# Kernel tuning notes

Measured on AMD Instinct MI355X. Metric: run time of the kernel, lower is better.

## Reference

```python
import jax, jax.numpy as jnp
import numpy as np

NUM_HEADS = 4
LN_EPS = 1e-5
NEG_INF = -1e9


def _ln(x, g, b):
    mu = jnp.mean(x, axis=-1, keepdims=True)
    var = jnp.mean(jnp.square(x - mu), axis=-1, keepdims=True)
    return (x - mu) * jax.lax.rsqrt(var + LN_EPS) * g + b


def setup_inputs() -> dict:
    key = jax.random.key(0)
    B, L, D, C, E, T, H, NL, MLP = 1024, 200, 64, 32, 32, 8, 256, 3, 256
    P = D + E            # 96
    KIN = H + 2 * T      # 272
    ks = iter(jax.random.split(key, 64))

    def w(shape, fan_in):
        return jax.random.normal(next(ks), shape, dtype=jnp.float32) / np.sqrt(fan_in)

    inp = {}
    inp['x_u'] = jax.random.normal(next(ks), (B, D), dtype=jnp.float32)
    inp['x_ctx'] = jax.random.normal(next(ks), (B, L, D), dtype=jnp.float32)
    inp['t_ctx'] = jax.random.uniform(next(ks), (B, L), dtype=jnp.float32)
    inp['act_u_idx'] = jax.random.randint(next(ks), (B,), 0, C + 1)
    inp['act_ctx_idx'] = jax.random.randint(next(ks), (B, L), 0, C + 1)
    emb = jax.random.normal(next(ks), (C + 1, E), dtype=jnp.float32)
    inp['emb'] = emb.at[0].set(0.0)  # padding_idx=0
    inp['W_in_self'] = w((P, H), P); inp['b_in_self'] = jnp.zeros((H,), jnp.float32)
    inp['W_in_ctx'] = w((P, H), P); inp['b_in_ctx'] = jnp.zeros((H,), jnp.float32)
    inp['freq'] = jax.random.normal(next(ks), (NL, T), dtype=jnp.float32)
    inp['phase'] = jnp.zeros((NL, T), jnp.float32)
    inp['Wq'] = w((NL, H, H), H)
    inp['Wk'] = w((NL, KIN, H), KIN)
    inp['Wv'] = w((NL, KIN, H), KIN)
    inp['Wres'] = w((NL, H, H), H); inp['bres'] = jnp.zeros((NL, H), jnp.float32)
    inp['Wff1'] = w((NL, H, H), H); inp['bff1'] = jnp.zeros((NL, H), jnp.float32)
    inp['Wff2'] = w((NL, H, H), H); inp['bff2'] = jnp.zeros((NL, H), jnp.float32)
    inp['g1'] = jnp.ones((NL, H), jnp.float32); inp['beta1'] = jnp.zeros((NL, H), jnp.float32)
    inp['g2'] = jnp.ones((NL, H), jnp.float32); inp['beta2'] = jnp.zeros((NL, H), jnp.float32)
    inp['W_ro'] = w((H, MLP), H); inp['b_ro'] = jnp.zeros((MLP,), jnp.float32)
    inp['W_cls'] = w((MLP, C), MLP); inp['b_cls'] = jnp.zeros((C,), jnp.float32)
    inp['W_dt'] = w((MLP, 1), MLP); inp['b_dt'] = jnp.zeros((1,), jnp.float32)
    inp['W_rem'] = w((MLP, 1), MLP); inp['b_rem'] = jnp.zeros((1,), jnp.float32)
    return inp


def reference(x_u, x_ctx, t_ctx, act_u_idx, act_ctx_idx, emb,
              W_in_self, b_in_self, W_in_ctx, b_in_ctx,
              freq, phase, Wq, Wk, Wv, Wres, bres,
              Wff1, bff1, Wff2, bff2, g1, beta1, g2, beta2,
              W_ro, b_ro, W_cls, b_cls, W_dt, b_dt, W_rem, b_rem):
    B, L, _ = x_ctx.shape
    H = W_in_self.shape[1]
    nh = NUM_HEADS
    Dh = H // nh
    scale = np.sqrt(Dh).astype(np.float32)

    mask = act_ctx_idx > 0                                   # (B, L)
    e_u = emb[act_u_idx]                                     # (B, E)
    e_ctx = emb[act_ctx_idx]                                 # (B, L, E)
    xu = jnp.concatenate([x_u, e_u], axis=-1)
    xc = jnp.concatenate([x_ctx, e_ctx], axis=-1)
    h = xu @ W_in_self + b_in_self                           # (B, H)
    ctx = xc @ W_in_ctx + b_in_ctx                           # (B, L, H)

    logt = jnp.log1p(jnp.maximum(t_ctx, 0.0))                # (B, L)
    n_layers = Wq.shape[0]
    for i in range(n_layers):
        z = logt[..., None] * freq[i] + phase[i]             # (B, L, T)
        te = jnp.concatenate([jnp.sin(z), jnp.cos(z)], axis=-1)  # (B, L, 2T)
        kv = jnp.concatenate([ctx, te], axis=-1)             # (B, L, H+2T)
        q = (h @ Wq[i]).reshape(B, nh, Dh)                   # (B, h, d)
        k = (kv @ Wk[i]).reshape(B, L, nh, Dh)               # (B, l, h, d)
        v = (kv @ Wv[i]).reshape(B, L, nh, Dh)
        att_logits = jnp.einsum('bhd,blhd->bhl', q, k) / scale
        att_logits = jnp.where(mask[:, None, :], att_logits, NEG_INF)
        att = jax.nn.softmax(att_logits, axis=-1)            # (B, h, l)
        agg = jnp.einsum('bhl,blhd->bhd', att, v).reshape(B, H)
        z1 = _ln(agg + h @ Wres[i] + bres[i], g1[i], beta1[i])
        ff = jax.nn.relu(z1 @ Wff1[i] + bff1[i]) @ Wff2[i] + bff2[i]
        h = _ln(z1 + ff, g2[i], beta2[i])

    z = jax.nn.relu(h @ W_ro + b_ro)
    logits = z @ W_cls + b_cls
    dt_hat = jax.nn.sigmoid(z @ W_dt + b_dt)
    rem_hat = jax.nn.sigmoid(z @ W_rem + b_rem)
    return (logits, dt_hat, rem_hat)
```

## Files before the change

kernel.cpp:

```cpp
#include <hip/hip_runtime.h>
#include <math.h>

namespace {
constexpr int Bc   = 1024;
constexpr int Lc   = 200;
constexpr int Dc   = 64;
constexpr int Ec   = 32;
constexpr int Pc   = 96;
constexpr int Hc   = 256;
constexpr int Tc   = 8;
constexpr int NLc  = 3;
constexpr int KINc = 272;
constexpr int DHc  = 64;
constexpr int Cc   = 32;
constexpr int QS   = 113;
constexpr int Q4   = 452;
constexpr int QP   = 464;
constexpr int CG   = 112;
constexpr int CGW  = 448;
constexpr int XROWS = Bc * Lc + 8;
constexpr int TEBS  = Bc * Lc + 8;
constexpr float LN_EPS_V = 1e-5f;
constexpr float NEG_BIG  = -1e9f;

typedef __attribute__((ext_vector_type(8))) short bf16x8;
typedef __attribute__((ext_vector_type(4))) float f32x4;

__device__ __forceinline__ unsigned short f2bf(float f) {
    union { float f; unsigned int u; } v; v.f = f;
    unsigned int u = v.u;
    unsigned int r = (u + 0x7fffu + ((u >> 16) & 1u)) >> 16;
    return (unsigned short)r;
}
}

__global__ __launch_bounds__(256) void k_kpv(const float* __restrict__ W_in_ctx,
                                             const float* __restrict__ b_in_ctx,
                                             const float* __restrict__ Wv,
                                             const float* __restrict__ Wk,
                                             float* __restrict__ wvp2,
                                             float* __restrict__ kp) {
    int blk = blockIdx.x;
    int i = blk / QS;
    int j = blk - i * QS;
    int t = threadIdx.x;
    __shared__ float wrow[Hc];
    if (j < 96)        wrow[t] = W_in_ctx[j * Hc + t];
    else if (j == 112) wrow[t] = b_in_ctx[t];
    __syncthreads();
    const float* WvL = Wv + (size_t)i * KINc * Hc;
    const float* WkL = Wk + (size_t)i * KINc * Hc;
    float av, ak;
    if (j >= 96 && j < 112) {
        av = WvL[(256 + (j - 96)) * Hc + t];
        ak = WkL[(256 + (j - 96)) * Hc + t];
    } else {
        av = 0.f; ak = 0.f;
        for (int c = 0; c < Hc; ++c) {
            float w = wrow[c];
            av += w * WvL[c * Hc + t];
            ak += w * WkL[c * Hc + t];
        }
    }
    wvp2[(size_t)blk * Hc + t] = av;
    kp[(size_t)blk * Hc + t]   = ak;
}

__global__ __launch_bounds__(256) void k_wbig2(const float* __restrict__ Wq,
                                               const float* __restrict__ kp,
                                               float* __restrict__ wbig) {
    __shared__ float wq_l[64][65];
    __shared__ float kp_l[113][64];
    int blk = blockIdx.x;
    int i = blk >> 4;
    int rem = blk & 15;
    int h = rem >> 2, et = rem & 3;
    int t = threadIdx.x;
    for (int idx = t; idx < 64 * 64; idx += 256) {
        int e = idx >> 6, d = idx & 63;
        wq_l[e][d] = Wq[(size_t)i * Hc * Hc + (size_t)(et * 64 + e) * Hc + h * 64 + d];
    }
    for (int idx = t; idx < 113 * 64; idx += 256) {
        int r = idx >> 6, d = idx & 63;
        kp_l[r][d] = kp[((size_t)i * QS + r) * Hc + h * 64 + d];
    }
    __syncthreads();
    int e  = t & 63;
    int rq = t >> 6;
    for (int r = rq; r < QS; r += 4) {
        float acc = 0.f;
        #pragma unroll
        for (int d = 0; d < 64; ++d) acc += wq_l[e][d] * kp_l[r][d];
        wbig[((size_t)i * Hc + et * 64 + e) * Q4 + h * QS + r] = 0.125f * acc;
    }
}

__global__ __launch_bounds__(64) void k_frag(const float* __restrict__ wvp2,
                                             const float* __restrict__ Wres,
                                             const float* __restrict__ Wff1,
                                             const float* __restrict__ Wff2,
                                             const float* __restrict__ wbig,
                                             unsigned short* __restrict__ wcatF,
                                             unsigned short* __restrict__ wffF,
                                             unsigned short* __restrict__ wbigF) {
    int blk = blockIdx.x;
    int lane = threadIdx.x;
    unsigned short v[8];
    if (blk < NLc * 352) {
        int i = blk / 352;
        int r = blk - i * 352;
        int kk = r >> 4, ct = r & 15;
        int c = ct * 16 + (lane & 15);
        int kb = kk * 32 + (lane >> 4) * 8;
        #pragma unroll
        for (int j = 0; j < 8; ++j) {
            int k = kb + j;
            float val;
            if (k < 448) {
                int hh = k / 112, jj = k - hh * 112;
                val = ((c >> 6) == hh) ? wvp2[((size_t)i * QS + jj) * Hc + c] : 0.f;
            } else {
                val = Wres[(size_t)i * Hc * Hc + (k - 448) * Hc + c];
            }
            v[j] = f2bf(val);
        }
        *(uint4*)&wcatF[(size_t)blk * 64 * 8 + lane * 8] = *(const uint4*)v;
    } else if (blk < NLc * 352 + NLc * 256) {
        int b2 = blk - NLc * 352;
        int i = b2 / 256;
        int rem = b2 - i * 256;
        int w12 = rem >> 7;
        int r = rem & 127;
        int kk = r >> 4, ct = r & 15;
        int c = ct * 16 + (lane & 15);
        int kb = kk * 32 + (lane >> 4) * 8;
        const float* src = (w12 ? Wff2 : Wff1) + (size_t)i * Hc * Hc;
        #pragma unroll
        for (int j = 0; j < 8; ++j) v[j] = f2bf(src[(size_t)(kb + j) * Hc + c]);
        *(uint4*)&wffF[(size_t)b2 * 64 * 8 + lane * 8] = *(const uint4*)v;
    } else {
        int b3 = blk - NLc * 352 - NLc * 256;
        int i = b3 / 232;
        int r = b3 - i * 232;
        int kk = r / 29, ct = r - kk * 29;
        int c = ct * 16 + (lane & 15);
        int kb = kk * 32 + (lane >> 4) * 8;
        #pragma unroll
        for (int j = 0; j < 8; ++j) {
            float val = (c < Q4) ? wbig[((size_t)i * Hc + kb + j) * Q4 + c] : 0.f;
            v[j] = f2bf(val);
        }
        *(uint4*)&wbigF[(size_t)b3 * 64 * 8 + lane * 8] = *(const uint4*)v;
    }
}

__global__ __launch_bounds__(256) void k_h0(const float* __restrict__ x_u,
                                            const int* __restrict__ act_u,
                                            const float* __restrict__ emb,
                                            const float* __restrict__ W,
                                            const float* __restrict__ bias,
                                            float* __restrict__ h) {
    constexpr int R = 16;
    int b0 = blockIdx.x * R;
    int t = threadIdx.x;
    __shared__ float xu[R * Pc];
    for (int idx = t; idx < R * Pc; idx += 256) {
        int r = idx / Pc, j = idx - r * Pc;
        int b = b0 + r;
        float v;
        if (j < Dc) v = x_u[b * Dc + j];
        else        v = emb[act_u[b] * Ec + (j - Dc)];
        xu[idx] = v;
    }
    __syncthreads();
    float acc[R];
    float bb = bias[t];
    #pragma unroll
    for (int r = 0; r < R; ++r) acc[r] = bb;
    for (int j = 0; j < Pc; ++j) {
        float w = W[j * Hc + t];
        #pragma unroll
        for (int r = 0; r < R; ++r) acc[r] += xu[r * Pc + j] * w;
    }
    #pragma unroll
    for (int r = 0; r < R; ++r) h[(b0 + r) * Hc + t] = acc[r];
}

__global__ __launch_bounds__(256) void k_prepx(const float* __restrict__ x_ctx,
                                               const int* __restrict__ act_ctx,
                                               const float* __restrict__ emb,
                                               unsigned short* __restrict__ xtb,
                                               unsigned short* __restrict__ xtTb) {
    constexpr int ST2 = 116;
    __shared__ __align__(16) unsigned short xsT[96 * ST2];
    int blk = blockIdx.x;
    int b  = blk >> 1;
    int h0 = blk & 1;
    int t = threadIdx.x;
    int wv = t >> 6, lane = t & 63;
    int m = lane & 15, kg = lane >> 4;

    bf16x8 ifrag[2];
    #pragma unroll
    for (int hh = 0; hh < 2; ++hh) {
        unsigned short v[8];
        #pragma unroll
        for (int j8 = 0; j8 < 8; ++j8)
            v[j8] = (kg * 8 + j8 == m + 16 * hh) ? (unsigned short)0x3F80u : (unsigned short)0;
        ifrag[hh] = *(const bf16x8*)v;
    }

    for (int tile = wv; tile < 7; tile += 4) {
        int l = h0 * 112 + tile * 16 + m;
        bool valid = l < Lc;
        bf16x8 afr[3];
        #pragma unroll
        for (int kk = 0; kk < 2; ++kk) {
            unsigned short tmp[8];
            if (valid) {
                const float* s = x_ctx + ((size_t)(b * Lc + l)) * Dc + kk * 32 + kg * 8;
                float4 a0 = *(const float4*)s;
                float4 a1 = *(const float4*)(s + 4);
                tmp[0]=f2bf(a0.x); tmp[1]=f2bf(a0.y); tmp[2]=f2bf(a0.z); tmp[3]=f2bf(a0.w);
                tmp[4]=f2bf(a1.x); tmp[5]=f2bf(a1.y); tmp[6]=f2bf(a1.z); tmp[7]=f2bf(a1.w);
            } else {
                #pragma unroll
                for (int j = 0; j < 8; ++j) tmp[j] = 0;
            }
            afr[kk] = *(const bf16x8*)tmp;
        }
        {
            unsigned short tmp[8];
            if (valid) {
                int a = act_ctx[b * Lc + l];
                const float* s = emb + (size_t)a * Ec + kg * 8;
                float4 e0 = *(const float4*)s;
                float4 e1 = *(const float4*)(s + 4);
                tmp[0]=f2bf(e0.x); tmp[1]=f2bf(e0.y); tmp[2]=f2bf(e0.z); tmp[3]=f2bf(e0.w);
                tmp[4]=f2bf(e1.x); tmp[5]=f2bf(e1.y); tmp[6]=f2bf(e1.z); tmp[7]=f2bf(e1.w);
            } else {
                #pragma unroll
                for (int j = 0; j < 8; ++j) tmp[j] = 0;
            }
            afr[2] = *(const bf16x8*)tmp;
        }
        if (valid) {
            unsigned short* dst = xtb + ((size_t)(b * Lc + l)) * 96;
            *(uint4*)(dst + kg * 8)      = *(const uint4*)&afr[0];
            *(uint4*)(dst + 32 + kg * 8) = *(const uint4*)&afr[1];
            *(uint4*)(dst + 64 + kg * 8) = *(const uint4*)&afr[2];
        }
        #pragma unroll
        for (int kk = 0; kk < 3; ++kk) {
            #pragma unroll
            for (int hh = 0; hh < 2; ++hh) {
                f32x4 d = {0.f, 0.f, 0.f, 0.f};
                d = __builtin_amdgcn_mfma_f32_16x16x32_bf16(afr[kk], ifrag[hh], d, 0, 0, 0);
                int j  = kk * 32 + hh * 16 + m;
                int l0 = tile * 16 + kg * 4;
                unsigned int u0 = (unsigned int)f2bf(d[0]) | ((unsigned int)f2bf(d[1]) << 16);
                unsigned int u1 = (unsigned int)f2bf(d[2]) | ((unsigned int)f2bf(d[3]) << 16);
                uint2 uu; uu.x = u0; uu.y = u1;
                *(uint2*)&xsT[j * ST2 + l0] = uu;
            }
        }
    }
    __syncthreads();

    for (int idx = t; idx < 96 * 14; idx += 256) {
        int j = idx / 14, ch = idx - j * 14;
        uint2 a  = *(const uint2*)&xsT[j * ST2 + ch * 8];
        uint2 b2 = *(const uint2*)&xsT[j * ST2 + ch * 8 + 4];
        uint4 o; o.x = a.x; o.y = a.y; o.z = b2.x; o.w = b2.y;
        *(uint4*)&xtTb[((size_t)(b * 96 + j)) * 224 + h0 * 112 + ch * 8] = o;
    }
}

__global__ __launch_bounds__(256) void k_prept(const float* __restrict__ t_ctx,
                                               const float* __restrict__ freq,
                                               const float* __restrict__ phase,
                                               unsigned short* __restrict__ teb,
                                               unsigned short* __restrict__ teTb) {
    __shared__ float lt[Lc];
    int b = blockIdx.x;
    int t = threadIdx.x;
    if (t < Lc) lt[t] = log1pf(fmaxf(t_ctx[b * Lc + t], 0.f));
    __syncthreads();
    for (int idx = t; idx < NLc * Lc; idx += 256) {
        int i = idx / Lc, l = idx - i * Lc;
        float L = lt[l];
        unsigned short v[16];
        #pragma unroll
        for (int j = 0; j < 8; ++j) {
            float z = L * freq[i * Tc + j] + phase[i * Tc + j];
            v[j]     = f2bf(__sinf(z));
            v[8 + j] = f2bf(__cosf(z));
        }
        size_t base = ((size_t)i * TEBS + b * Lc + l) * 16;
        *(uint4*)&teb[base]     = *(const uint4*)v;
        *(uint4*)&teb[base + 8] = *(const uint4*)&v[8];
    }
    for (int idx = t; idx < NLc * 16 * 28; idx += 256) {
        int i  = idx / 448;
        int r2 = idx - i * 448;
        int f  = r2 / 28, ch = r2 - f * 28;
        int l0 = ch * 8;
        float fr = freq[i * Tc + (f & 7)], ph = phase[i * Tc + (f & 7)];
        bool iscos = f >= 8;
        unsigned short v[8];
        #pragma unroll
        for (int k = 0; k < 8; ++k) {
            int l = l0 + k;
            float val = 0.f;
            if (l < Lc) {
                float z = lt[l] * fr + ph;
                val = iscos ? __cosf(z) : __sinf(z);
            }
            v[k] = f2bf(val);
        }
        *(uint4*)&teTb[((size_t)i * Bc * 16 + b * 16 + f) * 224 + l0] = *(const uint4*)v;
    }
}

__global__ __launch_bounds__(256) void k_qk2b(const float* __restrict__ h,
                                              const float* __restrict__ wbig_l,
                                              unsigned short* __restrict__ qk2b) {
    constexpr int R = 4;
    int rb = blockIdx.x & 255;
    int cb = blockIdx.x >> 8;
    int b0 = rb * R;
    int t = threadIdx.x;
    int c = cb * 256 + t;
    __shared__ float hl[R * Hc];
    for (int idx = t; idx < R * Hc; idx += 256) hl[idx] = h[b0 * Hc + idx];
    __syncthreads();
    if (c >= QP) return;
    if (c >= Q4) {
        #pragma unroll
        for (int r = 0; r < R; ++r) qk2b[(size_t)(b0 + r) * QP + c] = 0;
        return;
    }
    float acc[R];
    #pragma unroll
    for (int r = 0; r < R; ++r) acc[r] = 0.f;
    for (int e = 0; e < Hc; ++e) {
        float w = wbig_l[(size_t)e * Q4 + c];
        #pragma unroll
        for (int r = 0; r < R; ++r) acc[r] += hl[r * Hc + e] * w;
    }
    #pragma unroll
    for (int r = 0; r < R; ++r) qk2b[(size_t)(b0 + r) * QP + c] = f2bf(acc[r]);
}

__global__ __launch_bounds__(512) void k_att(const int* __restrict__ act_ctx,
                                             const unsigned short* __restrict__ qk2b,
                                             const unsigned short* __restrict__ xtb,
                                             const unsigned short* __restrict__ xtTb,
                                             const unsigned short* __restrict__ teb_l,
                                             const unsigned short* __restrict__ teTb_l,
                                             float* __restrict__ cagg) {
    __shared__ unsigned short qks[QP];
    __shared__ float S[4][208];
    __shared__ unsigned short Pl[16][232];
    int b = blockIdx.x;
    int t = threadIdx.x;
    int wv = t >> 6, lane = t & 63;
    int kg = lane >> 4;

    if (t < QP / 2) ((unsigned int*)qks)[t] = ((const unsigned int*)(qk2b + (size_t)b * QP))[t];
    for (int idx = t; idx < 16 * 29; idx += 512) {
        int row = idx / 29, c8 = idx - row * 29;
        uint4 z = {0, 0, 0, 0};
        *(uint4*)&Pl[row][c8 * 8] = z;
    }
    __syncthreads();

    bf16x8 bfr[4];
    {
        int h = lane & 15;
        int kb = kg * 8;
        #pragma unroll
        for (int kk = 0; kk < 4; ++kk) {
            unsigned short tmp[8];
            #pragma unroll
            for (int j = 0; j < 8; ++j) {
                int k = kk * 32 + kb + j;
                tmp[j] = (h < 4 && k < QS) ? qks[h * QS + k] : (unsigned short)0;
            }
            bfr[kk] = *(const bf16x8*)tmp;
        }
    }

    const unsigned short* xrow  = xtb   + (size_t)b * Lc * 96;
    const unsigned short* terow = teb_l + (size_t)b * Lc * 16;
    for (int tile = wv; tile < 13; tile += 8) {
        int r = tile * 16 + (lane & 15);
        bf16x8 a0 = *(const bf16x8*)(xrow + (size_t)r * 96 + kg * 8);
        bf16x8 a1 = *(const bf16x8*)(xrow + (size_t)r * 96 + 32 + kg * 8);
        bf16x8 a2 = *(const bf16x8*)(xrow + (size_t)r * 96 + 64 + kg * 8);
        bf16x8 a3;
        if (kg < 2) {
            a3 = *(const bf16x8*)(terow + (size_t)r * 16 + kg * 8);
        } else if (kg == 2) {
            unsigned short tmp[8] = {0x3F80u, 0, 0, 0, 0, 0, 0, 0};
            a3 = *(const bf16x8*)tmp;
        } else {
            bf16x8 z = {0, 0, 0, 0, 0, 0, 0, 0};
            a3 = z;
        }
        f32x4 acc = {0.f, 0.f, 0.f, 0.f};
        acc = __builtin_amdgcn_mfma_f32_16x16x32_bf16(a0, bfr[0], acc, 0, 0, 0);
        acc = __builtin_amdgcn_mfma_f32_16x16x32_bf16(a1, bfr[1], acc, 0, 0, 0);
        acc = __builtin_amdgcn_mfma_f32_16x16x32_bf16(a2, bfr[2], acc, 0, 0, 0);
        acc = __builtin_amdgcn_mfma_f32_16x16x32_bf16(a3, bfr[3], acc, 0, 0, 0);
        int h = lane & 15;
        if (h < 4) {
            int rb = tile * 16 + kg * 4;
            #pragma unroll
            for (int q = 0; q < 4; ++q) S[h][rb + q] = acc[q];
        }
    }
    __syncthreads();

    if (wv < 4) {
        int h = wv;
        float lv[4];
        #pragma unroll
        for (int k = 0; k < 4; ++k) {
            int l = lane + 64 * k;
            if (l < Lc) lv[k] = (act_ctx[b * Lc + l] > 0) ? S[h][l] : NEG_BIG;
            else        lv[k] = -INFINITY;
        }
        float m = fmaxf(fmaxf(lv[0], lv[1]), fmaxf(lv[2], lv[3]));
        #pragma unroll
        for (int off = 32; off >= 1; off >>= 1) m = fmaxf(m, __shfl_xor(m, off));
        float p[4];
        float ssum = 0.f;
        #pragma unroll
        for (int k = 0; k < 4; ++k) {
            int l = lane + 64 * k;
            p[k] = (l < Lc) ? __expf(lv[k] - m) : 0.f;
            ssum += p[k];
        }
        #pragma unroll
        for (int off = 32; off >= 1; off >>= 1) ssum += __shfl_xor(ssum, off);
        float sinv = 1.f / ssum;
        #pragma unroll
        for (int k = 0; k < 4; ++k) {
            int l = lane + 64 * k;
            if (l < Lc) Pl[wv][l] = f2bf(p[k] * sinv);
        }
    }
    __syncthreads();

    const unsigned short* xT  = xtTb   + (size_t)b * 96 * 224;
    const unsigned short* teT = teTb_l + (size_t)b * 16 * 224;
    if (wv < 7) {
        int tile = wv;
        int n = lane & 15;
        const unsigned short* brow = (tile < 6) ? (xT + ((size_t)(tile * 16 + n)) * 224)
                                                : (teT + (size_t)n * 224);
        f32x4 acc = {0.f, 0.f, 0.f, 0.f};
        #pragma unroll
        for (int kk = 0; kk < 7; ++kk) {
            bf16x8 a  = *(const bf16x8*)&Pl[lane & 15][kk * 32 + kg * 8];
            bf16x8 bb = *(const bf16x8*)(brow + kk * 32 + kg * 8);
            acc = __builtin_amdgcn_mfma_f32_16x16x32_bf16(a, bb, acc, 0, 0, 0);
        }
        if (kg == 0) {
            #pragma unroll
            for (int q = 0; q < 4; ++q)
                cagg[(size_t)b * CGW + q * CG + tile * 16 + n] = acc[q];
        }
    }
}

__global__ __launch_bounds__(512) void k_postq(const float* __restrict__ cagg,
                                               float* __restrict__ h,
                                               const float* __restrict__ wvp2L,
                                               const unsigned short* __restrict__ wcatF_l,
                                               const unsigned short* __restrict__ wff1F_l,
                                               const unsigned short* __restrict__ wff2F_l,
                                               const float* __restrict__ bresL,
                                               const float* __restrict__ bff1L,
                                               const float* __restrict__ bff2L,
                                               const float* __restrict__ g1L,
                                               const float* __restrict__ beta1L,
                                               const float* __restrict__ g2L,
                                               const float* __restrict__ beta2L,
                                               const unsigned short* __restrict__ wbigF_next,
                                               unsigned short* __restrict__ qk2b) {
    __shared__ __align__(16) unsigned short Xa[16 * 712];
    __shared__ float z1f[16 * 260];
    __shared__ __align__(16) unsigned short z1n[16 * 264];
    __shared__ __align__(16) unsigned short fb16[16 * 264];
    int r0 = blockIdx.x * 16;
    int t = threadIdx.x;
    int wv = t >> 6, lane = t & 63;
    int n = lane & 15, kg = lane >> 4;

    for (int idx = t; idx < 16 * 704; idx += 512) {
        int r = idx / 704, c = idx - r * 704;
        float v = (c < 448) ? cagg[(size_t)(r0 + r) * CGW + c]
                            : h[(size_t)(r0 + r) * Hc + (c - 448)];
        Xa[r * 712 + c] = f2bf(v);
    }
    __syncthreads();

    {
        f32x4 acc0 = {0.f,0.f,0.f,0.f}, acc1 = {0.f,0.f,0.f,0.f};
        for (int kk = 0; kk < 22; ++kk) {
            bf16x8 a = *(const bf16x8*)&Xa[(lane & 15) * 712 + kk * 32 + kg * 8];
            bf16x8 b0 = *(const bf16x8*)(wcatF_l + (((size_t)kk * 16 + wv * 2) * 64 + lane) * 8);
            bf16x8 b1 = *(const bf16x8*)(wcatF_l + (((size_t)kk * 16 + wv * 2 + 1) * 64 + lane) * 8);
            acc0 = __builtin_amdgcn_mfma_f32_16x16x32_bf16(a, b0, acc0, 0, 0, 0);
            acc1 = __builtin_amdgcn_mfma_f32_16x16x32_bf16(a, b1, acc1, 0, 0, 0);
        }
        int c0 = (wv * 2) * 16 + n, c1 = (wv * 2 + 1) * 16 + n;
        float bi0 = bresL[c0] + wvp2L[112 * Hc + c0];
        float bi1 = bresL[c1] + wvp2L[112 * Hc + c1];
        #pragma unroll
        for (int q = 0; q < 4; ++q) {
            z1f[(kg * 4 + q) * 260 + c0] = acc0[q] + bi0;
            z1f[(kg * 4 + q) * 260 + c1] = acc1[q] + bi1;
        }
    }
    __syncthreads();
    if (wv < 4) {
        int row = wv * 4 + kg;
        float sm = 0.f, sq = 0.f, vals[16];
        #pragma unroll
        for (int s = 0; s < 16; ++s) {
            float v = z1f[row * 260 + n + 16 * s];
            vals[s] = v; sm += v; sq += v * v;
        }
        #pragma unroll
        for (int off = 8; off >= 1; off >>= 1) { sm += __shfl_xor(sm, off); sq += __shfl_xor(sq, off); }
        float mu = sm * (1.f / 256.f);
        float rstd = rsqrtf(sq * (1.f / 256.f) - mu * mu + LN_EPS_V);
        #pragma unroll
        for (int s = 0; s < 16; ++s) {
            int c = n + 16 * s;
            float v = (vals[s] - mu) * rstd * g1L[c] + beta1L[c];
            z1f[row * 260 + c] = v;
            z1n[row * 264 + c] = f2bf(v);
        }
    }
    __syncthreads();
    {
        f32x4 acc0 = {0.f,0.f,0.f,0.f}, acc1 = {0.f,0.f,0.f,0.f};
        for (int kk = 0; kk < 8; ++kk) {
            bf16x8 a = *(const bf16x8*)&z1n[(lane & 15) * 264 + kk * 32 + kg * 8];
            bf16x8 b0 = *(const bf16x8*)(wff1F_l + (((size_t)kk * 16 + wv * 2) * 64 + lane) * 8);
            bf16x8 b1 = *(const bf16x8*)(wff1F_l + (((size_t)kk * 16 + wv * 2 + 1) * 64 + lane) * 8);
            acc0 = __builtin_amdgcn_mfma_f32_16x16x32_bf16(a, b0, acc0, 0, 0, 0);
            acc1 = __builtin_amdgcn_mfma_f32_16x16x32_bf16(a, b1, acc1, 0, 0, 0);
        }
        int c0 = (wv * 2) * 16 + n, c1 = (wv * 2 + 1) * 16 + n;
        float bi0 = bff1L[c0], bi1 = bff1L[c1];
        #pragma unroll
        for (int q = 0; q < 4; ++q) {
            fb16[(kg * 4 + q) * 264 + c0] = f2bf(fmaxf(acc0[q] + bi0, 0.f));
            fb16[(kg * 4 + q) * 264 + c1] = f2bf(fmaxf(acc1[q] + bi1, 0.f));
        }
    }
    __syncthreads();
    {
        f32x4 acc0 = {0.f,0.f,0.f,0.f}, acc1 = {0.f,0.f,0.f,0.f};
        for (int kk = 0; kk < 8; ++kk) {
            bf16x8 a = *(const bf16x8*)&fb16[(lane & 15) * 264 + kk * 32 + kg * 8];
            bf16x8 b0 = *(const bf16x8*)(wff2F_l + (((size_t)kk * 16 + wv * 2) * 64 + lane) * 8);
            bf16x8 b1 = *(const bf16x8*)(wff2F_l + (((size_t)kk * 16 + wv * 2 + 1) * 64 + lane) * 8);
            acc0 = __builtin_amdgcn_mfma_f32_16x16x32_bf16(a, b0, acc0, 0, 0, 0);
            acc1 = __builtin_amdgcn_mfma_f32_16x16x32_bf16(a, b1, acc1, 0, 0, 0);
        }
        int c0 = (wv * 2) * 16 + n, c1 = (wv * 2 + 1) * 16 + n;
        float bi0 = bff2L[c0], bi1 = bff2L[c1];
        #pragma unroll
        for (int q = 0; q < 4; ++q) {
            int row = kg * 4 + q;
            z1f[row * 260 + c0] = acc0[q] + bi0 + z1f[row * 260 + c0];
            z1f[row * 260 + c1] = acc1[q] + bi1 + z1f[row * 260 + c1];
        }
    }
    __syncthreads();
    if (wv < 4) {
        int row = wv * 4 + kg;
        float sm = 0.f, sq = 0.f, vals[16];
        #pragma unroll
        for (int s = 0; s < 16; ++s) {
            float v = z1f[row * 260 + n + 16 * s];
            vals[s] = v; sm += v; sq += v * v;
        }
        #pragma unroll
        for (int off = 8; off >= 1; off >>= 1) { sm += __shfl_xor(sm, off); sq += __shfl_xor(sq, off); }
        float mu = sm * (1.f / 256.f);
        float rstd = rsqrtf(sq * (1.f / 256.f) - mu * mu + LN_EPS_V);
        #pragma unroll
        for (int s = 0; s < 16; ++s) {
            int c = n + 16 * s;
            float v = (vals[s] - mu) * rstd * g2L[c] + beta2L[c];
            h[(size_t)(r0 + row) * Hc + c] = v;
            z1n[row * 264 + c] = f2bf(v);
        }
    }
    __syncthreads();
    if (wbigF_next) {
        for (int ct = wv; ct < 29; ct += 8) {
            f32x4 acc = {0.f, 0.f, 0.f, 0.f};
            for (int kk = 0; kk < 8; ++kk) {
                bf16x8 a = *(const bf16x8*)&z1n[(lane & 15) * 264 + kk * 32 + kg * 8];
                bf16x8 bb = *(const bf16x8*)(wbigF_next + (((size_t)kk * 29 + ct) * 64 + lane) * 8);
                acc = __builtin_amdgcn_mfma_f32_16x16x32_bf16(a, bb, acc, 0, 0, 0);
            }
            #pragma unroll
            for (int q = 0; q < 4; ++q)
                qk2b[(size_t)(r0 + kg * 4 + q) * QP + ct * 16 + n] = f2bf(acc[q]);
        }
    }
}

__global__ __launch_bounds__(256) void k_head(const float* __restrict__ h,
                                              const float* __restrict__ W_ro,
                                              const float* __restrict__ b_ro,
                                              const float* __restrict__ W_cls,
                                              const float* __restrict__ b_cls,
                                              const float* __restrict__ W_dt,
                                              const float* __restrict__ b_dt,
                                              const float* __restrict__ W_rem,
                                              const float* __restrict__ b_rem,
                                              float* __restrict__ out) {
    constexpr int R = 8;
    int b0 = blockIdx.x * R;
    int t = threadIdx.x;
    int wave = t >> 6, lane = t & 63;
    __shared__ float hl[R * Hc], zl[R * Hc];
    __shared__ float wcls[Hc * Cc];
    __shared__ float wdt[Hc], wrem[Hc];
    for (int idx = t; idx < R * Hc; idx += 256) hl[idx] = h[b0 * Hc + idx];
    for (int idx = t; idx < Hc * Cc; idx += 256) wcls[idx] = W_cls[idx];
    wdt[t] = W_dt[t];
    wrem[t] = W_rem[t];
    __syncthreads();
    float acc[R];
    float br = b_ro[t];
    #pragma unroll
    for (int r = 0; r < R; ++r) acc[r] = br;
    for (int d = 0; d < Hc; ++d) {
        float w = W_ro[d * Hc + t];
        #pragma unroll
        for (int r = 0; r < R; ++r) acc[r] += hl[r * Hc + d] * w;
    }
    #pragma unroll
    for (int r = 0; r < R; ++r) zl[r * Hc + t] = fmaxf(acc[r], 0.f);
    __syncthreads();
    {
        int rr = t >> 5;
        int c = t & 31;
        float a = b_cls[c];
        for (int d = 0; d < Hc; ++d) a += zl[rr * Hc + d] * wcls[d * Cc + c];
        out[(size_t)(b0 + rr) * Cc + c] = a;
    }
    for (int rr = wave * 2; rr < wave * 2 + 2; ++rr) {
        float sd = 0.f, sr = 0.f;
        #pragma unroll
        for (int k2 = 0; k2 < 4; ++k2) {
            float zv = zl[rr * Hc + lane + 64 * k2];
            sd += zv * wdt[lane + 64 * k2];
            sr += zv * wrem[lane + 64 * k2];
        }
        #pragma unroll
        for (int off = 32; off >= 1; off >>= 1) { sd += __shfl_xor(sd, off); sr += __shfl_xor(sr, off); }
        if (lane == 0) {
            out[(size_t)Bc * Cc + b0 + rr]      = 1.f / (1.f + __expf(-(sd + b_dt[0])));
            out[(size_t)Bc * Cc + Bc + b0 + rr] = 1.f / (1.f + __expf(-(sr + b_rem[0])));
        }
    }
}

extern "C" void kernel_launch(void* const* d_in, const int* in_sizes, int n_in,
                              void* d_out, int out_size, void* d_ws, size_t ws_size,
                              hipStream_t stream) {
    const float* x_u      = (const float*)d_in[0];
    const float* x_ctx    = (const float*)d_in[1];
    const float* t_ctx    = (const float*)d_in[2];
    const int*   act_u    = (const int*)d_in[3];
    const int*   act_ctx  = (const int*)d_in[4];
    const float* emb      = (const float*)d_in[5];
    const float* W_in_self = (const float*)d_in[6];
    const float* b_in_self = (const float*)d_in[7];
    const float* W_in_ctx  = (const float*)d_in[8];
    const float* b_in_ctx  = (const float*)d_in[9];
    const float* freq  = (const float*)d_in[10];
    const float* phase = (const float*)d_in[11];
    const float* Wq    = (const float*)d_in[12];
    const float* Wk    = (const float*)d_in[13];
    const float* Wv    = (const float*)d_in[14];
    const float* Wres  = (const float*)d_in[15];
    const float* bres  = (const float*)d_in[16];
    const float* Wff1  = (const float*)d_in[17];
    const float* bff1  = (const float*)d_in[18];
    const float* Wff2  = (const float*)d_in[19];
    const float* bff2  = (const float*)d_in[20];
    const float* g1    = (const float*)d_in[21];
    const float* beta1 = (const float*)d_in[22];
    const float* g2    = (const float*)d_in[23];
    const float* beta2 = (const float*)d_in[24];
    const float* W_ro  = (const float*)d_in[25];
    const float* b_ro  = (const float*)d_in[26];
    const float* W_cls = (const float*)d_in[27];
    const float* b_cls = (const float*)d_in[28];
    const float* W_dt  = (const float*)d_in[29];
    const float* b_dt  = (const float*)d_in[30];
    const float* W_rem = (const float*)d_in[31];
    const float* b_rem = (const float*)d_in[32];

    float* ws    = (float*)d_ws;
    float* hbuf  = ws;
    float* wbig  = hbuf  + (size_t)Bc * Hc;
    float* cagg2 = wbig  + (size_t)NLc * Hc * Q4;
    float* wvp2  = cagg2 + (size_t)Bc * CGW;
    float* kp    = wvp2  + (size_t)NLc * QS * Hc;
    unsigned short* xtb   = (unsigned short*)(kp + (size_t)NLc * QS * Hc);
    unsigned short* xtTb  = xtb   + (size_t)XROWS * 96;
    unsigned short* teb   = xtTb  + (size_t)Bc * 96 * 224;
    unsigned short* teTb  = teb   + (size_t)NLc * TEBS * 16;
    unsigned short* qk2b  = teTb  + (size_t)NLc * Bc * 16 * 224;
    unsigned short* wcatF = qk2b  + (size_t)Bc * QP;
    unsigned short* wffF  = wcatF + (size_t)NLc * 352 * 512;
    unsigned short* wbigF = wffF  + (size_t)NLc * 2 * 128 * 512;
    size_t need = ((size_t)Bc * Hc + (size_t)NLc * Hc * Q4
                  + (size_t)Bc * CGW + 2 * (size_t)NLc * QS * Hc) * 4
                + ((size_t)XROWS * 96 + (size_t)Bc * 96 * 224
                  + (size_t)NLc * TEBS * 16 + (size_t)NLc * Bc * 16 * 224
                  + (size_t)Bc * QP
                  + (size_t)NLc * 352 * 512 + (size_t)NLc * 2 * 128 * 512
                  + (size_t)NLc * 232 * 512) * 2;
    if (ws_size < need) return;

    float* out = (float*)d_out;

    k_kpv<<<NLc * QS, 256, 0, stream>>>(W_in_ctx, b_in_ctx, Wv, Wk, wvp2, kp);
    k_wbig2<<<NLc * 16, 256, 0, stream>>>(Wq, kp, wbig);
    k_frag<<<NLc * (352 + 256 + 232), 64, 0, stream>>>(wvp2, Wres, Wff1, Wff2, wbig,
                                                       wcatF, wffF, wbigF);
    k_h0<<<Bc / 16, 256, 0, stream>>>(x_u, act_u, emb, W_in_self, b_in_self, hbuf);
    k_prepx<<<Bc * 2, 256, 0, stream>>>(x_ctx, act_ctx, emb, xtb, xtTb);
    k_prept<<<Bc, 256, 0, stream>>>(t_ctx, freq, phase, teb, teTb);
    k_qk2b<<<512, 256, 0, stream>>>(hbuf, wbig, qk2b);

    for (int i = 0; i < NLc; ++i) {
        k_att<<<Bc, 512, 0, stream>>>(act_ctx, qk2b, xtb, xtTb,
                                      teb + (size_t)i * TEBS * 16,
                                      teTb + (size_t)i * Bc * 16 * 224, cagg2);
        const unsigned short* wbnext = (i < NLc - 1) ? (wbigF + (size_t)(i + 1) * 232 * 512)
                                                     : (const unsigned short*)nullptr;
        k_postq<<<Bc / 16, 512, 0, stream>>>(cagg2, hbuf,
                                             wvp2 + (size_t)i * QS * Hc,
                                             wcatF + (size_t)i * 352 * 512,
                                             wffF + (size_t)(i * 2) * 128 * 512,
                                             wffF + (size_t)(i * 2 + 1) * 128 * 512,
                                             bres + i * Hc, bff1 + i * Hc, bff2 + i * Hc,
                                             g1 + i * Hc, beta1 + i * Hc,
                                             g2 + i * Hc, beta2 + i * Hc,
                                             wbnext, qk2b);
    }
    k_head<<<Bc / 8, 256, 0, stream>>>(hbuf, W_ro, b_ro, W_cls, b_cls,
                                       W_dt, b_dt, W_rem, b_rem, out);
}
```

Baseline: 234.7 us.

## Drop transposed context copy; stage context rows in LDS inside attention

The preprocessing kernel no longer builds a second, transposed bf16 copy of the context features and becomes a simple elementwise convert-and-gather. Each attention block now loads its 200 context rows into shared memory once. It reads them row-wise for the key-side MFMA and column-wise (strided LDS gathers) for the value-side MFMA, replacing the global reads of both copies. This removes a large global write and a read stream each layer, at the cost of extra LDS (about 46KB more per block), which may lower occupancy, and slow scalar transposed LDS reads.

```diff
diff --git a/kernel.cpp b/kernel.cpp
--- a/kernel.cpp
+++ b/kernel.cpp
@@ -18,7 +18,6 @@
 constexpr int QP   = 464;
 constexpr int CG   = 112;
 constexpr int CGW  = 448;
-constexpr int XROWS = Bc * Lc + 8;
 constexpr int TEBS  = Bc * Lc + 8;
 constexpr float LN_EPS_V = 1e-5f;
 constexpr float NEG_BIG  = -1e9f;
@@ -189,91 +188,25 @@
 __global__ __launch_bounds__(256) void k_prepx(const float* __restrict__ x_ctx,
                                                const int* __restrict__ act_ctx,
                                                const float* __restrict__ emb,
-                                               unsigned short* __restrict__ xtb,
-                                               unsigned short* __restrict__ xtTb) {
-    constexpr int ST2 = 116;
-    __shared__ __align__(16) unsigned short xsT[96 * ST2];
-    int blk = blockIdx.x;
-    int b  = blk >> 1;
-    int h0 = blk & 1;
-    int t = threadIdx.x;
-    int wv = t >> 6, lane = t & 63;
-    int m = lane & 15, kg = lane >> 4;
-
-    bf16x8 ifrag[2];
-    #pragma unroll
-    for (int hh = 0; hh < 2; ++hh) {
-        unsigned short v[8];
-        #pragma unroll
-        for (int j8 = 0; j8 < 8; ++j8)
-            v[j8] = (kg * 8 + j8 == m + 16 * hh) ? (unsigned short)0x3F80u : (unsigned short)0;
-        ifrag[hh] = *(const bf16x8*)v;
-    }
-
-    for (int tile = wv; tile < 7; tile += 4) {
-        int l = h0 * 112 + tile * 16 + m;
-        bool valid = l < Lc;
-        bf16x8 afr[3];
-        #pragma unroll
-        for (int kk = 0; kk < 2; ++kk) {
-            unsigned short tmp[8];
-            if (valid) {
-                const float* s = x_ctx + ((size_t)(b * Lc + l)) * Dc + kk * 32 + kg * 8;
-                float4 a0 = *(const float4*)s;
-                float4 a1 = *(const float4*)(s + 4);
-                tmp[0]=f2bf(a0.x); tmp[1]=f2bf(a0.y); tmp[2]=f2bf(a0.z); tmp[3]=f2bf(a0.w);
-                tmp[4]=f2bf(a1.x); tmp[5]=f2bf(a1.y); tmp[6]=f2bf(a1.z); tmp[7]=f2bf(a1.w);
-            } else {
-                #pragma unroll
-                for (int j = 0; j < 8; ++j) tmp[j] = 0;
-            }
-            afr[kk] = *(const bf16x8*)tmp;
-        }
-        {
-            unsigned short tmp[8];
-            if (valid) {
-                int a = act_ctx[b * Lc + l];
-                const float* s = emb + (size_t)a * Ec + kg * 8;
-                float4 e0 = *(const float4*)s;
-                float4 e1 = *(const float4*)(s + 4);
-                tmp[0]=f2bf(e0.x); tmp[1]=f2bf(e0.y); tmp[2]=f2bf(e0.z); tmp[3]=f2bf(e0.w);
-                tmp[4]=f2bf(e1.x); tmp[5]=f2bf(e1.y); tmp[6]=f2bf(e1.z); tmp[7]=f2bf(e1.w);
-            } else {
-                #pragma unroll
-                for (int j = 0; j < 8; ++j) tmp[j] = 0;
-            }
-            afr[2] = *(const bf16x8*)tmp;
-        }
-        if (valid) {
-            unsigned short* dst = xtb + ((size_t)(b * Lc + l)) * 96;
-            *(uint4*)(dst + kg * 8)      = *(const uint4*)&afr[0];
-            *(uint4*)(dst + 32 + kg * 8) = *(const uint4*)&afr[1];
-            *(uint4*)(dst + 64 + kg * 8) = *(const uint4*)&afr[2];
-        }
-        #pragma unroll
-        for (int kk = 0; kk < 3; ++kk) {
-            #pragma unroll
-            for (int hh = 0; hh < 2; ++hh) {
-                f32x4 d = {0.f, 0.f, 0.f, 0.f};
-                d = __builtin_amdgcn_mfma_f32_16x16x32_bf16(afr[kk], ifrag[hh], d, 0, 0, 0);
-                int j  = kk * 32 + hh * 16 + m;
-                int l0 = tile * 16 + kg * 4;
-                unsigned int u0 = (unsigned int)f2bf(d[0]) | ((unsigned int)f2bf(d[1]) << 16);
-                unsigned int u1 = (unsigned int)f2bf(d[2]) | ((unsigned int)f2bf(d[3]) << 16);
-                uint2 uu; uu.x = u0; uu.y = u1;
-                *(uint2*)&xsT[j * ST2 + l0] = uu;
-            }
-        }
-    }
-    __syncthreads();
-
-    for (int idx = t; idx < 96 * 14; idx += 256) {
-        int j = idx / 14, ch = idx - j * 14;
-        uint2 a  = *(const uint2*)&xsT[j * ST2 + ch * 8];
-        uint2 b2 = *(const uint2*)&xsT[j * ST2 + ch * 8 + 4];
-        uint4 o; o.x = a.x; o.y = a.y; o.z = b2.x; o.w = b2.y;
-        *(uint4*)&xtTb[((size_t)(b * 96 + j)) * 224 + h0 * 112 + ch * 8] = o;
-    }
+                                               unsigned short* __restrict__ xtb) {
+    int idx = blockIdx.x * 256 + threadIdx.x;
+    int row = idx / 12, c8 = idx - row * 12;
+    unsigned short v[8];
+    if (c8 < 8) {
+        const float* s = x_ctx + (size_t)row * Dc + c8 * 8;
+        float4 a0 = *(const float4*)s;
+        float4 a1 = *(const float4*)(s + 4);
+        v[0]=f2bf(a0.x); v[1]=f2bf(a0.y); v[2]=f2bf(a0.z); v[3]=f2bf(a0.w);
+        v[4]=f2bf(a1.x); v[5]=f2bf(a1.y); v[6]=f2bf(a1.z); v[7]=f2bf(a1.w);
+    } else {
+        int a = act_ctx[row];
+        const float* s = emb + (size_t)a * Ec + (c8 - 8) * 8;
+        float4 e0 = *(const float4*)s;
+        float4 e1 = *(const float4*)(s + 4);
+        v[0]=f2bf(e0.x); v[1]=f2bf(e0.y); v[2]=f2bf(e0.z); v[3]=f2bf(e0.w);
+        v[4]=f2bf(e1.x); v[5]=f2bf(e1.y); v[6]=f2bf(e1.z); v[7]=f2bf(e1.w);
+    }
+    *(uint4*)&xtb[(size_t)row * 96 + c8 * 8] = *(const uint4*)v;
 }
 
 __global__ __launch_bounds__(256) void k_prept(const float* __restrict__ t_ctx,
@@ -355,10 +288,11 @@
 __global__ __launch_bounds__(512) void k_att(const int* __restrict__ act_ctx,
                                              const unsigned short* __restrict__ qk2b,
                                              const unsigned short* __restrict__ xtb,
-                                             const unsigned short* __restrict__ xtTb,
                                              const unsigned short* __restrict__ teb_l,
                                              const unsigned short* __restrict__ teTb_l,
                                              float* __restrict__ cagg) {
+    constexpr int XS = 112;
+    __shared__ __align__(16) unsigned short xt[208 * XS];
     __shared__ unsigned short qks[QP];
     __shared__ float S[4][208];
     __shared__ unsigned short Pl[16][232];
@@ -372,6 +306,17 @@
         int row = idx / 29, c8 = idx - row * 29;
         uint4 z = {0, 0, 0, 0};
         *(uint4*)&Pl[row][c8 * 8] = z;
+    }
+    const unsigned short* xrow = xtb + (size_t)b * Lc * 96;
+    for (int idx = t; idx < Lc * 12; idx += 512) {
+        int l = idx / 12, c8 = idx - l * 12;
+        uint4 v = *(const uint4*)(xrow + (size_t)l * 96 + c8 * 8);
+        *(uint4*)&xt[l * XS + c8 * 8] = v;
+    }
+    for (int idx = t; idx < 8 * 12; idx += 512) {
+        int l = 200 + idx / 12, c8 = idx - (idx / 12) * 12;
+        uint4 z = {0, 0, 0, 0};
+        *(uint4*)&xt[l * XS + c8 * 8] = z;
     }
     __syncthreads();
 
@@ -391,13 +336,12 @@
         }
     }
 
-    const unsigned short* xrow  = xtb   + (size_t)b * Lc * 96;
     const unsigned short* terow = teb_l + (size_t)b * Lc * 16;
     for (int tile = wv; tile < 13; tile += 8) {
         int r = tile * 16 + (lane & 15);
-        bf16x8 a0 = *(const bf16x8*)(xrow + (size_t)r * 96 + kg * 8);
-        bf16x8 a1 = *(const bf16x8*)(xrow + (size_t)r * 96 + 32 + kg * 8);
-        bf16x8 a2 = *(const bf16x8*)(xrow + (size_t)r * 96 + 64 + kg * 8);
+        bf16x8 a0 = *(const bf16x8*)&xt[r * XS + kg * 8];
+        bf16x8 a1 = *(const bf16x8*)&xt[r * XS + 32 + kg * 8];
+        bf16x8 a2 = *(const bf16x8*)&xt[r * XS + 64 + kg * 8];
         bf16x8 a3;
         if (kg < 2) {
             a3 = *(const bf16x8*)(terow + (size_t)r * 16 + kg * 8);
@@ -453,18 +397,24 @@
     }
     __syncthreads();
 
-    const unsigned short* xT  = xtTb   + (size_t)b * 96 * 224;
     const unsigned short* teT = teTb_l + (size_t)b * 16 * 224;
     if (wv < 7) {
         int tile = wv;
         int n = lane & 15;
-        const unsigned short* brow = (tile < 6) ? (xT + ((size_t)(tile * 16 + n)) * 224)
-                                                : (teT + (size_t)n * 224);
         f32x4 acc = {0.f, 0.f, 0.f, 0.f};
         #pragma unroll
         for (int kk = 0; kk < 7; ++kk) {
-            bf16x8 a  = *(const bf16x8*)&Pl[lane & 15][kk * 32 + kg * 8];
-            bf16x8 bb = *(const bf16x8*)(brow + kk * 32 + kg * 8);
+            bf16x8 a = *(const bf16x8*)&Pl[lane & 15][kk * 32 + kg * 8];
+            bf16x8 bb;
+            if (tile < 6) {
+                unsigned short tmp[8];
+                #pragma unroll
+                for (int jj = 0; jj < 8; ++jj)
+                    tmp[jj] = xt[(kk * 32 + kg * 8 + jj) * XS + tile * 16 + n];
+                bb = *(const bf16x8*)tmp;
+            } else {
+                bb = *(const bf16x8*)(teT + (size_t)n * 224 + kk * 32 + kg * 8);
+            }
             acc = __builtin_amdgcn_mfma_f32_16x16x32_bf16(a, bb, acc, 0, 0, 0);
         }
         if (kg == 0) {
@@ -722,8 +672,7 @@
     float* wvp2  = cagg2 + (size_t)Bc * CGW;
     float* kp    = wvp2  + (size_t)NLc * QS * Hc;
     unsigned short* xtb   = (unsigned short*)(kp + (size_t)NLc * QS * Hc);
-    unsigned short* xtTb  = xtb   + (size_t)XROWS * 96;
-    unsigned short* teb   = xtTb  + (size_t)Bc * 96 * 224;
+    unsigned short* teb   = xtb   + (size_t)Bc * Lc * 96;
     unsigned short* teTb  = teb   + (size_t)NLc * TEBS * 16;
     unsigned short* qk2b  = teTb  + (size_t)NLc * Bc * 16 * 224;
     unsigned short* wcatF = qk2b  + (size_t)Bc * QP;
@@ -731,7 +680,7 @@
     unsigned short* wbigF = wffF  + (size_t)NLc * 2 * 128 * 512;
     size_t need = ((size_t)Bc * Hc + (size_t)NLc * Hc * Q4
                   + (size_t)Bc * CGW + 2 * (size_t)NLc * QS * Hc) * 4
-                + ((size_t)XROWS * 96 + (size_t)Bc * 96 * 224
+                + ((size_t)Bc * Lc * 96
                   + (size_t)NLc * TEBS * 16 + (size_t)NLc * Bc * 16 * 224
                   + (size_t)Bc * QP
                   + (size_t)NLc * 352 * 512 + (size_t)NLc * 2 * 128 * 512
@@ -745,12 +694,12 @@
     k_frag<<<NLc * (352 + 256 + 232), 64, 0, stream>>>(wvp2, Wres, Wff1, Wff2, wbig,
                                                        wcatF, wffF, wbigF);
     k_h0<<<Bc / 16, 256, 0, stream>>>(x_u, act_u, emb, W_in_self, b_in_self, hbuf);
-    k_prepx<<<Bc * 2, 256, 0, stream>>>(x_ctx, act_ctx, emb, xtb, xtTb);
+    k_prepx<<<(Bc * Lc * 12) / 256, 256, 0, stream>>>(x_ctx, act_ctx, emb, xtb);
     k_prept<<<Bc, 256, 0, stream>>>(t_ctx, freq, phase, teb, teTb);
     k_qk2b<<<512, 256, 0, stream>>>(hbuf, wbig, qk2b);
 
     for (int i = 0; i < NLc; ++i) {
-        k_att<<<Bc, 512, 0, stream>>>(act_ctx, qk2b, xtb, xtTb,
+        k_att<<<Bc, 512, 0, stream>>>(act_ctx, qk2b, xtb,
                                       teb + (size_t)i * TEBS * 16,
                                       teTb + (size_t)i * Bc * 16 * 224, cagg2);
         const unsigned short* wbnext = (i < NLc - 1) ? (wbigF + (size_t)(i + 1) * 232 * 512)
```

Measured after the change: 235.0 us. About the same (+0.1%).
